# Kernel optimization log

Measured on AMD Instinct MI355X. Metric: run time of the kernel, lower is better.

Reference implementation:

```python
import jax, jax.numpy as jnp
import numpy as np

ALPHA = 0.25
GAMMA = 2.0
S_NORM = 4.0   # args.s_norm
E_EF = 0.2     # effective-box shrink factor
E_IG = 0.5     # ignoring-box shrink factor
LEVELS = [3, 4, 5, 6, 7]
B, A, K, H, W = 16, 16, 80, 1024, 1024


def _grids():
    xs, ys, lv = [], [], []
    for li, l in enumerate(LEVELS):
        s = 2 ** l
        fh, fw = (H + s - 1) // s, (W + s - 1) // s
        yy, xx = np.meshgrid(np.arange(fh), np.arange(fw), indexing='ij')
        xs.append(xx.ravel()); ys.append(yy.ravel()); lv.append(np.full(fh * fw, li))
    return (np.concatenate(xs).astype(np.int32),
            np.concatenate(ys).astype(np.int32),
            np.concatenate(lv).astype(np.int32))


def setup_inputs() -> dict:
    key = jax.random.key(0)
    k1, k2, k3, k4, k5, k6 = jax.random.split(key, 6)
    xg, yg, pr = _grids()  # P = 21824
    P = xg.shape[0]
    classifications = jax.random.uniform(k1, (B, P, K), jnp.float32, 0.01, 0.99)
    regressions = jax.random.uniform(k2, (B, P, 4), jnp.float32, 0.1, 8.0)
    x1 = jax.random.uniform(k3, (B, A), jnp.float32, 0.0, W - 96.0)
    y1 = jax.random.uniform(k4, (B, A), jnp.float32, 0.0, H - 96.0)
    bwh = jax.random.uniform(k5, (B, A, 2), jnp.float32, 48.0, 256.0)
    x2 = jnp.minimum(x1 + bwh[..., 0], W - 1.0)
    y2 = jnp.minimum(y1 + bwh[..., 1], H - 1.0)
    cls = jax.random.randint(k6, (B, A), 0, K).astype(jnp.float32)
    annotations = jnp.stack([x1, y1, x2, y2, cls], axis=-1)  # [B,A,5], all valid
    image = jnp.zeros((B, 3, H, W), jnp.float32)  # only shape is used
    return {"classifications": classifications, "regressions": regressions,
            "annotations": annotations, "image": image,
            "x_grid_order": jnp.asarray(xg), "y_grid_order": jnp.asarray(yg),
            "pyramid_reset": jnp.asarray(pr)}


def reference(classifications, regressions, annotations, image,
              x_grid_order, y_grid_order, pyramid_reset):
    strides = jnp.array([2.0 ** l for l in LEVELS], jnp.float32)  # [5]
    xg, yg, lev = x_grid_order, y_grid_order, pyramid_reset
    xf, yf = xg.astype(jnp.float32), yg.astype(jnp.float32)
    Kc = classifications.shape[-1]

    def fl(v):  # torch .long() on non-negative floats == floor
        return jnp.floor(v).astype(jnp.int32)

    def per_image(c, r, ann):
        boxes, cid = ann[:, :4], ann[:, 4].astype(jnp.int32)
        s = strides[None, :, None]
        proj = jnp.floor((boxes[:, None, :] + s - 1.0) / s)  # [A,5,4] box projections per level
        pw = proj[..., 2] - proj[..., 0]
        ph = proj[..., 3] - proj[..., 1]
        def shrink(e):
            f = (1.0 - e) / 2.0
            return jnp.stack([proj[..., 0] + f * pw, proj[..., 1] + f * ph,
                              proj[..., 2] - f * pw, proj[..., 3] - f * ph], axis=-1)
        eff, ign = shrink(E_EF), shrink(E_IG)
        # gather each pixel's own pyramid-level box coords -> [A,P,4]
        eff_p, ign_p, proj_p = eff[:, lev, :], ign[:, lev, :], proj[:, lev, :]
        m_eff = ((xg >= fl(eff_p[..., 0])) & (xg <= fl(eff_p[..., 2] + 1.0)) &
                 (yg >= fl(eff_p[..., 1])) & (yg <= fl(eff_p[..., 3] + 1.0)))  # [A,P]
        m_ign = ((xg >= fl(ign_p[..., 0] + 1.0)) & (xg <= fl(ign_p[..., 2])) &
                 (yg >= fl(ign_p[..., 1] + 1.0)) & (yg <= fl(ign_p[..., 3])))
        oh = jax.nn.one_hot(cid, Kc, dtype=jnp.float32)  # [A,K]
        eff_cov = jnp.einsum('ap,ak->pk', m_eff.astype(jnp.float32), oh) > 0
        ign_cov = jnp.einsum('ap,ak->pk', m_ign.astype(jnp.float32), oh) > 0
        # effective scatter (=1) overwrites ignoring scatter (=-1), else 0
        targets = jnp.where(eff_cov, 1.0, jnp.where(ign_cov, -1.0, 0.0))  # [P,K]
        nA = m_eff.shape[0]
        last = nA - 1 - jnp.argmax(m_eff[::-1], axis=0)  # [P]
        pb = jnp.take_along_axis(proj_p, last[None, :, None], axis=0)[0]  # [P,4]
        t_reg = jnp.stack([xf - pb[:, 0], pb[:, 2] - xf,
                           yf - pb[:, 1], pb[:, 3] - yf], axis=1) / S_NORM  # [P,4]
        x_gt = (t_reg[:, 2] + t_reg[:, 3] + 1.0) * (t_reg[:, 0] + t_reg[:, 1] + 1.0)
        x_pr = (r[:, 2] + r[:, 3] + 1.0) * (r[:, 0] + r[:, 1] + 1.0)
        i_h = jnp.minimum(t_reg[:, 2], r[:, 2]) + jnp.minimum(t_reg[:, 3], r[:, 3]) + 1.0
        i_w = jnp.minimum(t_reg[:, 0], r[:, 0]) + jnp.minimum(t_reg[:, 1], r[:, 1]) + 1.0
        inter = i_h * i_w
        iou = jnp.clip(inter / (x_pr + x_gt - inter), 1e-4, 1.0 - 1e-4)
        reg_l = -jnp.log(iou)  # [P]
        # focal classification loss
        cc = jnp.clip(c, 1e-4, 1.0 - 1e-4)
        pos = targets == 1.0
        af = jnp.where(pos, ALPHA, 1.0 - ALPHA)
        fwt = jnp.where(pos, 1.0 - cc, cc)
        bce = -(targets * jnp.log(cc) + (1.0 - targets) * jnp.log(1.0 - cc))
        cls_l = jnp.where(targets != -1.0, af * fwt ** GAMMA * bce, 0.0)
        wgt = pos.astype(jnp.float32)  # mean over (pixel,class) positive pairs
        n_eff = wgt.sum()
        cls_loss = cls_l.sum() / jnp.maximum(n_eff, 1.0)
        reg_loss = jnp.where(n_eff > 0,
                             (wgt * reg_l[:, None]).sum() / jnp.maximum(n_eff, 1.0), 0.0)
        return cls_loss, reg_loss

    cl, rl = jax.vmap(per_image)(classifications, regressions, annotations)
    return jnp.stack([cl.mean(), rl.mean()])
```

## Files before the change

### kernel.cpp

```cpp
#include <hip/hip_runtime.h>
#include <cstdint>

#define BB   16
#define AA   16
#define KK   80
#define NLEV 5
#define PP   21824

#define POS_PER_BLK 128
#define NBLK_X ((PP + POS_PER_BLK - 1) / POS_PER_BLK)

__device__ __forceinline__ void compute_bounds(float x1, float y1, float x2, float y2,
                                               float s, int* o, float* q)
{
#pragma clang fp contract(off)
    float p0 = floorf((x1 + s - 1.0f) / s);
    float p1 = floorf((y1 + s - 1.0f) / s);
    float p2 = floorf((x2 + s - 1.0f) / s);
    float p3 = floorf((y2 + s - 1.0f) / s);
    float pw = p2 - p0, ph = p3 - p1;
    float e0 = p0 + 0.4f * pw,  e1 = p1 + 0.4f * ph;
    float e2 = p2 - 0.4f * pw,  e3 = p3 - 0.4f * ph;
    float i0 = p0 + 0.25f * pw, i1 = p1 + 0.25f * ph;
    float i2 = p2 - 0.25f * pw, i3 = p3 - 0.25f * ph;
    o[0] = (int)floorf(e0);
    o[1] = (int)floorf(e2 + 1.0f);
    o[2] = (int)floorf(e1);
    o[3] = (int)floorf(e3 + 1.0f);
    o[4] = (int)floorf(i0 + 1.0f);
    o[5] = (int)floorf(i2);
    o[6] = (int)floorf(i1 + 1.0f);
    o[7] = (int)floorf(i3);
    q[0] = p0; q[1] = p1; q[2] = p2; q[3] = p3;
}

__device__ __forceinline__ float focal_term(float c, unsigned int em,
                                            unsigned int im, unsigned int cm)
{
    float cc  = fminf(fmaxf(c, 1e-4f), 1.0f - 1e-4f);
    bool  pos = (em & cm) != 0;
    bool  ign = (!pos) && ((im & cm) != 0);
    float arg = pos ? cc : (1.0f - cc);
    float fwt = 1.0f - arg;
    float af  = pos ? 0.25f : 0.75f;
    float l   = af * fwt * fwt * (-__logf(arg));
    return ign ? 0.0f : l;
}

__global__ void __launch_bounds__(256)
fused_kernel(const float4* __restrict__ cls4,
             const float4* __restrict__ reg4,
             const float* __restrict__ ann,
             const int* __restrict__ xg, const int* __restrict__ yg,
             const int* __restrict__ lev,
             float* __restrict__ pc, float* __restrict__ pr,
             int* __restrict__ pn)
{
    __shared__ int   sb[AA * NLEV * 8];
    __shared__ float sp[AA * NLEV * 4];
    __shared__ int   scid[AA];
    __shared__ uint4 scm[KK / 4];
    __shared__ unsigned int smask[POS_PER_BLK];
    __shared__ float swc[4], swr[4];
    __shared__ int   swn[4];

    const int  b    = blockIdx.y;
    const int  t    = threadIdx.x;
    const int  p0   = blockIdx.x * POS_PER_BLK;
    const bool full = (blockIdx.x < NBLK_X - 1);
    const int  npos = full ? POS_PER_BLK : (PP - (NBLK_X - 1) * POS_PER_BLK);

    const float* annb = ann + b * AA * 5;

    float bx0 = 0, bx1 = 0, bx2 = 0, bx3 = 0, cid1 = 0;
    float cidv[AA];
    if (t < AA * NLEV) {
        int a = t / NLEV;
        bx0 = annb[a * 5 + 0]; bx1 = annb[a * 5 + 1];
        bx2 = annb[a * 5 + 2]; bx3 = annb[a * 5 + 3];
    } else if (t >= 128 && t < 128 + KK) {
#pragma unroll
        for (int a = 0; a < AA; ++a) cidv[a] = annb[a * 5 + 4];
    } else if (t >= 224 && t < 224 + AA) {
        cid1 = annb[(t - 224) * 5 + 4];
    }

    const int pidx = p0 + ((t < npos) ? t : 0);
    int    x  = xg[pidx], y = yg[pidx], li = lev[pidx];
    float4 r4 = reg4[(size_t)b * PP + pidx];

    const int V = PP * KK / 4;
    const float4* cbase = cls4 + (size_t)b * V + (size_t)p0 * (KK / 4);
    float4 c0[10];
    if (full) {
#pragma unroll
        for (int u = 0; u < 10; ++u) c0[u] = cbase[t + 256 * u];
    } else {
#pragma unroll
        for (int u = 0; u < 5; ++u)  c0[u] = cbase[t + 256 * u];
    }

    if (t < AA * NLEV) {
        int l = t % NLEV;
        compute_bounds(bx0, bx1, bx2, bx3, (float)(8 << l), &sb[t * 8], &sp[t * 4]);
    } else if (t >= 128 && t < 128 + KK) {
        int k = t - 128;
        unsigned int m = 0;
#pragma unroll
        for (int a = 0; a < AA; ++a)
            if ((int)cidv[a] == k) m |= (1u << a);
        ((unsigned int*)scm)[k] = m;
    } else if (t >= 224 && t < 224 + AA) {
        scid[t - 224] = (int)cid1;
    }
    __syncthreads();

    float my_r = 0.0f; int my_n = 0;
    if (t < npos) {
        unsigned int em = 0, im = 0;
        for (int a = 0; a < AA; ++a) {
            const int* o = &sb[(a * NLEV + li) * 8];
            int me = (x >= o[0]) & (x <= o[1]) & (y >= o[2]) & (y <= o[3]);
            int mi = (x >= o[4]) & (x <= o[5]) & (y >= o[6]) & (y <= o[7]);
            em |= (unsigned int)me << a;
            im |= (unsigned int)mi << a;
        }
        smask[t] = em | (im << 16);

        unsigned long long lo = 0; unsigned int hi = 0;
        unsigned int m = em;
        while (m) {
            int a = __ffs(m) - 1; m &= m - 1;
            int c = scid[a];
            if (c < 64) lo |= 1ull << c; else hi |= 1u << (c - 64);
        }
        int np = __popcll(lo) + __popc(hi);

        int last = em ? (31 - __clz(em)) : (AA - 1);
        const float* pb = &sp[(last * NLEV + li) * 4];
        float xf = (float)x, yf = (float)y;
        float t0 = (xf - pb[0]) * 0.25f;
        float t1 = (pb[2] - xf) * 0.25f;
        float t2 = (yf - pb[1]) * 0.25f;
        float t3 = (pb[3] - yf) * 0.25f;
        float x_gt = (t2 + t3 + 1.0f) * (t0 + t1 + 1.0f);
        float x_pr = (r4.z + r4.w + 1.0f) * (r4.x + r4.y + 1.0f);
        float ih = fminf(t2, r4.z) + fminf(t3, r4.w) + 1.0f;
        float iw = fminf(t0, r4.x) + fminf(t1, r4.y) + 1.0f;
        float inter = ih * iw;
        float iou = inter / (x_pr + x_gt - inter);
        iou = fminf(fmaxf(iou, 1e-4f), 1.0f - 1e-4f);
        my_r = -logf(iou) * (float)np;
        my_n = np;
    }
    __syncthreads();

    float acc = 0.0f;
    if (full) {
#pragma unroll
        for (int u = 0; u < 10; ++u) {
            unsigned int il = (unsigned int)(t + 256 * u);
            unsigned int pl = il / 20u, k4 = il - pl * 20u;
            unsigned int mk = smask[pl];
            unsigned int em = mk & 0xFFFFu, im = mk >> 16;
            uint4 cm = scm[k4];
            acc += focal_term(c0[u].x, em, im, cm.x)
                 + focal_term(c0[u].y, em, im, cm.y)
                 + focal_term(c0[u].z, em, im, cm.z)
                 + focal_term(c0[u].w, em, im, cm.w);
        }
    } else {
#pragma unroll
        for (int u = 0; u < 5; ++u) {
            unsigned int il = (unsigned int)(t + 256 * u);
            unsigned int pl = il / 20u, k4 = il - pl * 20u;
            unsigned int mk = smask[pl];
            unsigned int em = mk & 0xFFFFu, im = mk >> 16;
            uint4 cm = scm[k4];
            acc += focal_term(c0[u].x, em, im, cm.x)
                 + focal_term(c0[u].y, em, im, cm.y)
                 + focal_term(c0[u].z, em, im, cm.z)
                 + focal_term(c0[u].w, em, im, cm.w);
        }
    }

    for (int off = 32; off > 0; off >>= 1) {
        acc  += __shfl_down(acc,  off);
        my_r += __shfl_down(my_r, off);
        my_n += __shfl_down(my_n, off);
    }
    int lane = t & 63, wv = t >> 6;
    if (lane == 0) { swc[wv] = acc; swr[wv] = my_r; swn[wv] = my_n; }
    __syncthreads();
    if (t == 0) {
        int slot = b * NBLK_X + blockIdx.x;
        pc[slot] = swc[0] + swc[1] + swc[2] + swc[3];
        pr[slot] = swr[0] + swr[1] + swr[2] + swr[3];
        pn[slot] = swn[0] + swn[1] + swn[2] + swn[3];
    }
}

__global__ void final_kernel(const float* __restrict__ pc,
                             const float* __restrict__ pr,
                             const int* __restrict__ pn,
                             float* __restrict__ out)
{
    __shared__ float sc[BB], sr[BB];
    int t = threadIdx.x;
    int b = t >> 4, chunk = t & 15;
    float cs = 0.0f, rs = 0.0f; int ns = 0;
    for (int i = chunk; i < NBLK_X; i += 16) {
        cs += pc[b * NBLK_X + i];
        rs += pr[b * NBLK_X + i];
        ns += pn[b * NBLK_X + i];
    }
    for (int off = 8; off > 0; off >>= 1) {
        cs += __shfl_down(cs, off, 16);
        rs += __shfl_down(rs, off, 16);
        ns += __shfl_down(ns, off, 16);
    }
    if (chunk == 0) {
        float d = fmaxf((float)ns, 1.0f);
        sc[b] = cs / d;
        sr[b] = (ns > 0) ? (rs / d) : 0.0f;
    }
    __syncthreads();
    if (t == 0) {
        float C = 0.0f, R = 0.0f;
        for (int i = 0; i < BB; ++i) { C += sc[i]; R += sr[i]; }
        out[0] = C * (1.0f / BB);
        out[1] = R * (1.0f / BB);
    }
}

extern "C" void kernel_launch(void* const* d_in, const int* in_sizes, int n_in,
                              void* d_out, int out_size, void* d_ws, size_t ws_size,
                              hipStream_t stream)
{
    const float* cls = (const float*)d_in[0];
    const float* reg = (const float*)d_in[1];
    const float* ann = (const float*)d_in[2];
    const int* xg = (const int*)d_in[4];
    const int* yg = (const int*)d_in[5];
    const int* lv = (const int*)d_in[6];
    float* out = (float*)d_out;

    char* ws = (char*)d_ws;
    float* pc = (float*)(ws + 0);
    float* pr = (float*)(ws + 12288);
    int*   pn = (int*)(ws + 24576);

    dim3 grid(NBLK_X, BB);
    fused_kernel<<<grid, 256, 0, stream>>>((const float4*)cls, (const float4*)reg,
                                           ann, xg, yg, lv, pc, pr, pn);

    final_kernel<<<1, 256, 0, stream>>>(pc, pr, pn, out);
}
```

Baseline: 314.6 us.

## Split fused loss kernel into mask pass and streaming focal pass via global masks

Splits the fused kernel in two. A small mask kernel writes the per-pixel effective and ignore bitmasks and the per-class masks to workspace, and it also computes the regression partials. A separate focal kernel then streams the classification tensor in flat chunks of 2048 float4 per block, reading those masks back. This removes the mask computation and its barrier from the critical path of the bandwidth-bound classification stream. The cost is an extra launch and a global round-trip of about 1.4 MB of masks.

Result: slower. 325.2 us (+3.4%).

```diff
diff --git a/kernel.cpp b/kernel.cpp
--- a/kernel.cpp
+++ b/kernel.cpp
@@ -8,7 +8,13 @@
 #define PP   21824
 
 #define POS_PER_BLK 128
-#define NBLK_X ((PP + POS_PER_BLK - 1) / POS_PER_BLK)
+#define NBLK_A ((PP + POS_PER_BLK - 1) / POS_PER_BLK)
+
+#define VV   (PP * KK / 4)
+#define UB   8
+#define CHUNK (256 * UB)
+#define NBLK_B ((VV + CHUNK - 1) / CHUNK)
+
 
 __device__ __forceinline__ void compute_bounds(float x1, float y1, float x2, float y2,
                                                float s, int* o, float* q)
@@ -48,37 +54,36 @@
 }
 
 __global__ void __launch_bounds__(256)
-fused_kernel(const float4* __restrict__ cls4,
-             const float4* __restrict__ reg4,
-             const float* __restrict__ ann,
-             const int* __restrict__ xg, const int* __restrict__ yg,
-             const int* __restrict__ lev,
-             float* __restrict__ pc, float* __restrict__ pr,
-             int* __restrict__ pn)
+mask_kernel(const float4* __restrict__ reg4,
+            const float* __restrict__ ann,
+            const int* __restrict__ xg, const int* __restrict__ yg,
+            const int* __restrict__ lev,
+            unsigned int* __restrict__ smask_g,
+            unsigned int* __restrict__ scm_g,
+            float* __restrict__ pr, int* __restrict__ pn)
 {
     __shared__ int   sb[AA * NLEV * 8];
     __shared__ float sp[AA * NLEV * 4];
     __shared__ int   scid[AA];
-    __shared__ uint4 scm[KK / 4];
-    __shared__ unsigned int smask[POS_PER_BLK];
-    __shared__ float swc[4], swr[4];
+    __shared__ float swr[4];
     __shared__ int   swn[4];
 
     const int  b    = blockIdx.y;
     const int  t    = threadIdx.x;
     const int  p0   = blockIdx.x * POS_PER_BLK;
-    const bool full = (blockIdx.x < NBLK_X - 1);
-    const int  npos = full ? POS_PER_BLK : (PP - (NBLK_X - 1) * POS_PER_BLK);
+    const bool full = (blockIdx.x < NBLK_A - 1);
+    const int  npos = full ? POS_PER_BLK : (PP - (NBLK_A - 1) * POS_PER_BLK);
 
     const float* annb = ann + b * AA * 5;
 
     float bx0 = 0, bx1 = 0, bx2 = 0, bx3 = 0, cid1 = 0;
     float cidv[AA];
+    const bool do_scm = (blockIdx.x == 0) && (t >= 128) && (t < 128 + KK);
     if (t < AA * NLEV) {
         int a = t / NLEV;
         bx0 = annb[a * 5 + 0]; bx1 = annb[a * 5 + 1];
         bx2 = annb[a * 5 + 2]; bx3 = annb[a * 5 + 3];
-    } else if (t >= 128 && t < 128 + KK) {
+    } else if (do_scm) {
 #pragma unroll
         for (int a = 0; a < AA; ++a) cidv[a] = annb[a * 5 + 4];
     } else if (t >= 224 && t < 224 + AA) {
@@ -89,27 +94,16 @@
     int    x  = xg[pidx], y = yg[pidx], li = lev[pidx];
     float4 r4 = reg4[(size_t)b * PP + pidx];
 
-    const int V = PP * KK / 4;
-    const float4* cbase = cls4 + (size_t)b * V + (size_t)p0 * (KK / 4);
-    float4 c0[10];
-    if (full) {
-#pragma unroll
-        for (int u = 0; u < 10; ++u) c0[u] = cbase[t + 256 * u];
-    } else {
-#pragma unroll
-        for (int u = 0; u < 5; ++u)  c0[u] = cbase[t + 256 * u];
-    }
-
     if (t < AA * NLEV) {
         int l = t % NLEV;
         compute_bounds(bx0, bx1, bx2, bx3, (float)(8 << l), &sb[t * 8], &sp[t * 4]);
-    } else if (t >= 128 && t < 128 + KK) {
+    } else if (do_scm) {
         int k = t - 128;
         unsigned int m = 0;
 #pragma unroll
         for (int a = 0; a < AA; ++a)
             if ((int)cidv[a] == k) m |= (1u << a);
-        ((unsigned int*)scm)[k] = m;
+        scm_g[b * KK + k] = m;
     } else if (t >= 224 && t < 224 + AA) {
         scid[t - 224] = (int)cid1;
     }
@@ -125,7 +119,7 @@
             em |= (unsigned int)me << a;
             im |= (unsigned int)mi << a;
         }
-        smask[t] = em | (im << 16);
+        smask_g[(size_t)b * PP + pidx] = em | (im << 16);
 
         unsigned long long lo = 0; unsigned int hi = 0;
         unsigned int m = em;
@@ -153,51 +147,74 @@
         my_r = -logf(iou) * (float)np;
         my_n = np;
     }
-    __syncthreads();
-
-    float acc = 0.0f;
-    if (full) {
-#pragma unroll
-        for (int u = 0; u < 10; ++u) {
-            unsigned int il = (unsigned int)(t + 256 * u);
-            unsigned int pl = il / 20u, k4 = il - pl * 20u;
-            unsigned int mk = smask[pl];
-            unsigned int em = mk & 0xFFFFu, im = mk >> 16;
-            uint4 cm = scm[k4];
-            acc += focal_term(c0[u].x, em, im, cm.x)
-                 + focal_term(c0[u].y, em, im, cm.y)
-                 + focal_term(c0[u].z, em, im, cm.z)
-                 + focal_term(c0[u].w, em, im, cm.w);
-        }
-    } else {
-#pragma unroll
-        for (int u = 0; u < 5; ++u) {
-            unsigned int il = (unsigned int)(t + 256 * u);
-            unsigned int pl = il / 20u, k4 = il - pl * 20u;
-            unsigned int mk = smask[pl];
-            unsigned int em = mk & 0xFFFFu, im = mk >> 16;
-            uint4 cm = scm[k4];
-            acc += focal_term(c0[u].x, em, im, cm.x)
-                 + focal_term(c0[u].y, em, im, cm.y)
-                 + focal_term(c0[u].z, em, im, cm.z)
-                 + focal_term(c0[u].w, em, im, cm.w);
-        }
-    }
 
     for (int off = 32; off > 0; off >>= 1) {
-        acc  += __shfl_down(acc,  off);
         my_r += __shfl_down(my_r, off);
         my_n += __shfl_down(my_n, off);
     }
     int lane = t & 63, wv = t >> 6;
-    if (lane == 0) { swc[wv] = acc; swr[wv] = my_r; swn[wv] = my_n; }
+    if (lane == 0) { swr[wv] = my_r; swn[wv] = my_n; }
     __syncthreads();
     if (t == 0) {
-        int slot = b * NBLK_X + blockIdx.x;
-        pc[slot] = swc[0] + swc[1] + swc[2] + swc[3];
+        int slot = b * NBLK_A + blockIdx.x;
         pr[slot] = swr[0] + swr[1] + swr[2] + swr[3];
         pn[slot] = swn[0] + swn[1] + swn[2] + swn[3];
     }
+}
+
+__global__ void __launch_bounds__(256)
+focal_kernel(const float4* __restrict__ cls4,
+             const unsigned int* __restrict__ smask_g,
+             const uint4* __restrict__ scm_g,
+             float* __restrict__ pc)
+{
+    __shared__ uint4        s_scm[KK / 4];
+    __shared__ unsigned int s_mk[112];
+    __shared__ float        swc[4];
+
+    const int b  = blockIdx.y;
+    const int bx = blockIdx.x;
+    const int t  = threadIdx.x;
+    const int base  = bx * CHUNK;
+    const int pl_lo = base / 20;
+
+    if (t < KK / 4) s_scm[t] = scm_g[b * (KK / 4) + t];
+    const int cnt = min(112, PP - pl_lo);
+    if (t >= 32 && (t - 32) < cnt)
+        s_mk[t - 32] = smask_g[(size_t)b * PP + pl_lo + (t - 32)];
+    __syncthreads();
+
+    float4 c4[UB];
+    const float4* cb = cls4 + (size_t)b * VV + base;
+#pragma unroll
+    for (int u = 0; u < UB; ++u) {
+        int off = t + 256 * u;
+        if (base + off < VV) c4[u] = cb[off];
+    }
+
+    float acc = 0.0f;
+#pragma unroll
+    for (int u = 0; u < UB; ++u) {
+        int off = base + t + 256 * u;
+        if (off < VV) {
+            unsigned int uoff = (unsigned int)off;
+            unsigned int pl = uoff / 20u;
+            unsigned int k4 = uoff - pl * 20u;
+            unsigned int mk = s_mk[pl - (unsigned int)pl_lo];
+            unsigned int em = mk & 0xFFFFu, im = mk >> 16;
+            uint4 cm = s_scm[k4];
+            acc += focal_term(c4[u].x, em, im, cm.x)
+                 + focal_term(c4[u].y, em, im, cm.y)
+                 + focal_term(c4[u].z, em, im, cm.z)
+                 + focal_term(c4[u].w, em, im, cm.w);
+        }
+    }
+
+    for (int off = 32; off > 0; off >>= 1) acc += __shfl_down(acc, off);
+    if ((t & 63) == 0) swc[t >> 6] = acc;
+    __syncthreads();
+    if (t == 0)
+        pc[b * NBLK_B + bx] = swc[0] + swc[1] + swc[2] + swc[3];
 }
 
 __global__ void final_kernel(const float* __restrict__ pc,
@@ -209,10 +226,10 @@
     int t = threadIdx.x;
     int b = t >> 4, chunk = t & 15;
     float cs = 0.0f, rs = 0.0f; int ns = 0;
-    for (int i = chunk; i < NBLK_X; i += 16) {
-        cs += pc[b * NBLK_X + i];
-        rs += pr[b * NBLK_X + i];
-        ns += pn[b * NBLK_X + i];
+    for (int i = chunk; i < NBLK_B; i += 16) cs += pc[b * NBLK_B + i];
+    for (int i = chunk; i < NBLK_A; i += 16) {
+        rs += pr[b * NBLK_A + i];
+        ns += pn[b * NBLK_A + i];
     }
     for (int off = 8; off > 0; off >>= 1) {
         cs += __shfl_down(cs, off, 16);
@@ -246,13 +263,19 @@
     float* out = (float*)d_out;
 
     char* ws = (char*)d_ws;
-    float* pc = (float*)(ws + 0);
-    float* pr = (float*)(ws + 12288);
-    int*   pn = (int*)(ws + 24576);
-
-    dim3 grid(NBLK_X, BB);
-    fused_kernel<<<grid, 256, 0, stream>>>((const float4*)cls, (const float4*)reg,
-                                           ann, xg, yg, lv, pc, pr, pn);
+    unsigned int* scm   = (unsigned int*)(ws + 0);
+    unsigned int* smask = (unsigned int*)(ws + 5120);
+    float* pr = (float*)(ws + 1401856);
+    int*   pn = (int*)(ws + 1412800);
+    float* pc = (float*)(ws + 1423744);
+
+    dim3 gridA(NBLK_A, BB);
+    mask_kernel<<<gridA, 256, 0, stream>>>((const float4*)reg, ann, xg, yg, lv,
+                                           smask, scm, pr, pn);
+
+    dim3 gridB(NBLK_B, BB);
+    focal_kernel<<<gridB, 256, 0, stream>>>((const float4*)cls, smask,
+                                            (const uint4*)scm, pc);
 
     final_kernel<<<1, 256, 0, stream>>>(pc, pr, pn, out);
 }
```
